# Optimization experiments

Measured on AMD Instinct MI355X. Metric: run time of the kernel, lower is better.

Reference implementation:

```python
import jax, jax.numpy as jnp
import numpy as np

N_NODES = 100000
N_EDGES = 1250000
IN_CH = 64
HID = 64
OUT_CH = 8
N_GRAPHS = 512


def _gcn_conv(x, W, b, src, dst, n):
    """PyG GCNConv: add self-loops, symmetric deg^-1/2 normalization, scatter-add."""
    h = x @ W  # [N, F_out]
    ones = jnp.ones(src.shape, dtype=h.dtype)
    deg = jax.ops.segment_sum(ones, dst, num_segments=n) + 1.0  # +1 for self-loop
    dinv = jax.lax.rsqrt(deg)
    coef = (dinv[src] * dinv[dst])[:, None]          # [E,1]
    agg = jax.ops.segment_sum(h[src] * coef, dst, num_segments=n)  # neighbor msgs
    self_term = h * (dinv * dinv)[:, None]           # self-loop msg, norm = 1/deg
    return agg + self_term + b


def setup_inputs() -> dict:
    key = jax.random.key(0)
    ks = jax.random.split(key, 8)
    x = jax.random.normal(ks[0], (N_NODES, IN_CH), dtype=jnp.float32)
    edge_index = jax.random.randint(ks[1], (2, N_EDGES), 0, N_NODES, dtype=jnp.int64)
    batch = jnp.sort(jax.random.randint(ks[2], (N_NODES,), 0, N_GRAPHS, dtype=jnp.int64))
    s = 0.1
    W0 = jax.random.normal(ks[3], (IN_CH, HID), dtype=jnp.float32) * s
    W1 = jax.random.normal(ks[4], (HID, HID), dtype=jnp.float32) * s
    W2 = jax.random.normal(ks[5], (HID, HID), dtype=jnp.float32) * s
    Wfc = jax.random.normal(ks[6], (HID, OUT_CH), dtype=jnp.float32) * s
    b0 = jnp.zeros((HID,), dtype=jnp.float32)
    b1 = jnp.zeros((HID,), dtype=jnp.float32)
    b2 = jnp.zeros((HID,), dtype=jnp.float32)
    bfc = jnp.zeros((OUT_CH,), dtype=jnp.float32)
    return {"x": x, "edge_index": edge_index, "batch": batch,
            "W0": W0, "b0": b0, "W1": W1, "b1": b1, "W2": W2, "b2": b2,
            "Wfc": Wfc, "bfc": bfc}


def reference(x, edge_index, batch, W0, b0, W1, b1, W2, b2, Wfc, bfc):
    src, dst = edge_index[0], edge_index[1]
    n = x.shape[0]
    h = jax.nn.relu(_gcn_conv(x, W0, b0, src, dst, n))
    h = jax.nn.relu(_gcn_conv(h, W1, b1, src, dst, n))
    h = jax.nn.relu(_gcn_conv(h, W2, b2, src, dst, n))
    # global_mean_pool over graph ids
    sums = jax.ops.segment_sum(h, batch, num_segments=N_GRAPHS)  # [G, HID]
    cnt = jax.ops.segment_sum(jnp.ones((n,), dtype=h.dtype), batch, num_segments=N_GRAPHS)
    pooled = sums / jnp.maximum(cnt, 1.0)[:, None]
    return jax.nn.sigmoid(pooled @ Wfc + bfc)  # [G, OUT_CH]
```

## Files before the change

kernel.cpp:

```cpp
#include <hip/hip_runtime.h>
#include <math.h>


#define FEAT 64
#define CAP 64
#define EDGE_BLOCKS 1024

typedef _Float16 half4 __attribute__((ext_vector_type(4)));
typedef float floatx2 __attribute__((ext_vector_type(2)));


__global__ void k_zero(int* __restrict__ p, int n, float* __restrict__ q, int m) {
    int i = blockIdx.x * blockDim.x + threadIdx.x;
    if (i < n) p[i] = 0;
    if (i < m) q[i] = 0.f;
}


__global__ void k_scatter(const int* __restrict__ ei, int* __restrict__ ecnt,
                          int* __restrict__ csr, int E, int N) {
    int g = blockIdx.x & 7;
    int bi = blockIdx.x >> 3;
    int lo = (int)((long long)N * g >> 3);
    int hi = (int)((long long)N * (g + 1) >> 3);
    for (int base = bi * 1024; base < E; base += (EDGE_BLOCKS / 8) * 1024) {
        int e0 = base + threadIdx.x;
        #pragma unroll
        for (int k = 0; k < 4; ++k) {
            int e = e0 + k * 256;
            if (e < E) {
                int s = ei[e];
                int d = ei[E + e];
                if (d >= lo && d < hi) {
                    int slot = atomicAdd(&ecnt[d], 1);
                    if (slot < CAP) csr[((size_t)d << 6) + slot] = s;
                }
            }
        }
    }
}


template<typename T>
__global__ __launch_bounds__(256, 2)
void k_matmul(const T* __restrict__ X, const float* __restrict__ W,
              const int* __restrict__ ecnt, unsigned int* __restrict__ h8,
              int n) {
    __shared__ float Ws[FEAT][68];
    __shared__ float Xs[FEAT][68];
    int tid = threadIdx.x;
    int cidx = tid & 15;
    int ridx = tid >> 4;
    int rowbase = blockIdx.x << 6;

    const float4* Wg4 = (const float4*)W;
    for (int idx = tid; idx < FEAT * 16; idx += 256) {
        int k = idx >> 4, p = idx & 15;
        *(float4*)&Ws[k][p << 2] = Wg4[idx];
    }
    for (int idx = tid; idx < FEAT * 16; idx += 256) {
        int r = idx >> 4, p = idx & 15;
        int row = rowbase + r;
        float4 v = make_float4(0.f, 0.f, 0.f, 0.f);
        if (row < n) {
            if constexpr (sizeof(T) == 4) {
                v = ((const float4*)X)[(size_t)row * 16 + p];
            } else {
                half4 hv = ((const half4*)X)[(size_t)row * 16 + p];
                v = make_float4((float)hv.x, (float)hv.y, (float)hv.z, (float)hv.w);
            }
        }
        *(float4*)&Xs[r][p << 2] = v;
    }
    __syncthreads();

    int r0 = ridx << 2;
    int c0 = cidx << 2;
    float4 a0 = make_float4(0.f, 0.f, 0.f, 0.f);
    float4 a1 = a0, a2 = a0, a3 = a0;
    #pragma unroll 2
    for (int k = 0; k < FEAT; k += 4) {
        float4 w0 = *(const float4*)&Ws[k + 0][c0];
        float4 w1 = *(const float4*)&Ws[k + 1][c0];
        float4 w2 = *(const float4*)&Ws[k + 2][c0];
        float4 w3 = *(const float4*)&Ws[k + 3][c0];
        float4 x0 = *(const float4*)&Xs[r0 + 0][k];
        float4 x1 = *(const float4*)&Xs[r0 + 1][k];
        float4 x2 = *(const float4*)&Xs[r0 + 2][k];
        float4 x3 = *(const float4*)&Xs[r0 + 3][k];
        a0.x += x0.x*w0.x + x0.y*w1.x + x0.z*w2.x + x0.w*w3.x;
        a0.y += x0.x*w0.y + x0.y*w1.y + x0.z*w2.y + x0.w*w3.y;
        a0.z += x0.x*w0.z + x0.y*w1.z + x0.z*w2.z + x0.w*w3.z;
        a0.w += x0.x*w0.w + x0.y*w1.w + x0.z*w2.w + x0.w*w3.w;
        a1.x += x1.x*w0.x + x1.y*w1.x + x1.z*w2.x + x1.w*w3.x;
        a1.y += x1.x*w0.y + x1.y*w1.y + x1.z*w2.y + x1.w*w3.y;
        a1.z += x1.x*w0.z + x1.y*w1.z + x1.z*w2.z + x1.w*w3.z;
        a1.w += x1.x*w0.w + x1.y*w1.w + x1.z*w2.w + x1.w*w3.w;
        a2.x += x2.x*w0.x + x2.y*w1.x + x2.z*w2.x + x2.w*w3.x;
        a2.y += x2.x*w0.y + x2.y*w1.y + x2.z*w2.y + x2.w*w3.y;
        a2.z += x2.x*w0.z + x2.y*w1.z + x2.z*w2.z + x2.w*w3.z;
        a2.w += x2.x*w0.w + x2.y*w1.w + x2.z*w2.w + x2.w*w3.w;
        a3.x += x3.x*w0.x + x3.y*w1.x + x3.z*w2.x + x3.w*w3.x;
        a3.y += x3.x*w0.y + x3.y*w1.y + x3.z*w2.y + x3.w*w3.y;
        a3.z += x3.x*w0.z + x3.y*w1.z + x3.z*w2.z + x3.w*w3.z;
        a3.w += x3.x*w0.w + x3.y*w1.w + x3.z*w2.w + x3.w*w3.w;
    }
    int row0 = rowbase + r0;
    #pragma unroll
    for (int r = 0; r < 4; ++r) {
        int row = row0 + r;
        if (row < n) {
            float4 a = (r == 0) ? a0 : (r == 1) ? a1 : (r == 2) ? a2 : a3;
            float dv = rsqrtf((float)ecnt[row] + 1.0f);
            unsigned int p = 0;
            p = __builtin_amdgcn_cvt_pk_fp8_f32(a.x * dv, a.y * dv, p, false);
            p = __builtin_amdgcn_cvt_pk_fp8_f32(a.z * dv, a.w * dv, p, true);
            h8[(size_t)row * 16 + cidx] = p;
        }
    }
}


__global__ void k_agg(const int* __restrict__ ecnt, const int* __restrict__ csr,
                      const unsigned int* __restrict__ h8,
                      const float* __restrict__ b, _Float16* __restrict__ out, int N) {
    int wid = (blockIdx.x * blockDim.x + threadIdx.x) >> 6;
    int lane = threadIdx.x & 63;
    int half = lane >> 5;
    int lanein = lane & 31;
    int eslot = lanein >> 4;
    int fq = lanein & 15;
    int node = wid * 2 + half;
    if (node >= N) return;
    int deg = ecnt[node];
    int off0 = node << 6;
    int e1 = off0 + deg;
    float4 acc = make_float4(0.f, 0.f, 0.f, 0.f);
    int j = off0 + eslot;
    for (; j + 2 < e1; j += 4) {
        unsigned int u0 = h8[(size_t)csr[j] * 16 + fq];
        unsigned int u1 = h8[(size_t)csr[j + 2] * 16 + fq];
        floatx2 l0 = __builtin_amdgcn_cvt_pk_f32_fp8(u0, false);
        floatx2 h0 = __builtin_amdgcn_cvt_pk_f32_fp8(u0, true);
        floatx2 l1 = __builtin_amdgcn_cvt_pk_f32_fp8(u1, false);
        floatx2 h1 = __builtin_amdgcn_cvt_pk_f32_fp8(u1, true);
        acc.x += l0.x + l1.x;
        acc.y += l0.y + l1.y;
        acc.z += h0.x + h1.x;
        acc.w += h0.y + h1.y;
    }
    if (j < e1) {
        unsigned int u = h8[(size_t)csr[j] * 16 + fq];
        floatx2 l = __builtin_amdgcn_cvt_pk_f32_fp8(u, false);
        floatx2 hh = __builtin_amdgcn_cvt_pk_f32_fp8(u, true);
        acc.x += l.x; acc.y += l.y; acc.z += hh.x; acc.w += hh.y;
    }
    acc.x += __shfl_xor(acc.x, 16); acc.y += __shfl_xor(acc.y, 16);
    acc.z += __shfl_xor(acc.z, 16); acc.w += __shfl_xor(acc.w, 16);
    if (eslot == 0) {
        unsigned int uo = h8[(size_t)node * 16 + fq];
        floatx2 ol = __builtin_amdgcn_cvt_pk_f32_fp8(uo, false);
        floatx2 oh = __builtin_amdgcn_cvt_pk_f32_fp8(uo, true);
        float4 bb = *(const float4*)&b[fq << 2];
        float dv = rsqrtf((float)deg + 1.0f);
        half4 r;
        r.x = (_Float16)fmaxf(dv * (acc.x + ol.x) + bb.x, 0.f);
        r.y = (_Float16)fmaxf(dv * (acc.y + ol.y) + bb.y, 0.f);
        r.z = (_Float16)fmaxf(dv * (acc.z + oh.x) + bb.z, 0.f);
        r.w = (_Float16)fmaxf(dv * (acc.w + oh.y) + bb.w, 0.f);
        *(half4*)&out[(size_t)node * FEAT + (fq << 2)] = r;
    }
}


#define PCH 64
__global__ void k_pool(const _Float16* __restrict__ h, const int* __restrict__ batch,
                       float* __restrict__ pooled, float* __restrict__ gcnt, int N) {
    int wave = blockIdx.x * (blockDim.x >> 6) + (threadIdx.x >> 6);
    int f = threadIdx.x & 63;
    int start = wave * PCH;
    if (start >= N) return;
    int end = start + PCH; if (end > N) end = N;
    int cur = batch[start];
    float acc = 0.f;
    int nl = 0;
    for (int i = start; i < end; ++i) {
        int g = batch[i];
        if (g != cur) {
            atomicAdd(&pooled[(size_t)cur * FEAT + f], acc);
            if (f == 0) atomicAdd(&gcnt[cur], (float)nl);
            cur = g; acc = 0.f; nl = 0;
        }
        acc += (float)h[(size_t)i * FEAT + f];
        nl++;
    }
    atomicAdd(&pooled[(size_t)cur * FEAT + f], acc);
    if (f == 0) atomicAdd(&gcnt[cur], (float)nl);
}

__global__ void k_fc_sigmoid(const float* __restrict__ pooled, const float* __restrict__ gcnt,
                             const float* __restrict__ Wfc, const float* __restrict__ bfc,
                             float* __restrict__ out, int G) {
    __shared__ float P[FEAT];
    int g = blockIdx.x;
    int t = threadIdx.x;
    float c = fmaxf(gcnt[g], 1.0f);
    P[t] = pooled[(size_t)g * FEAT + t] / c;
    __syncthreads();
    if (t < 8) {
        float acc = bfc[t];
        #pragma unroll
        for (int f = 0; f < FEAT; ++f) acc += P[f] * Wfc[f * 8 + t];
        out[(size_t)g * 8 + t] = 1.f / (1.f + expf(-acc));
    }
}


extern "C" void kernel_launch(void* const* d_in, const int* in_sizes, int n_in,
                              void* d_out, int out_size, void* d_ws, size_t ws_size,
                              hipStream_t stream) {
    const float* x    = (const float*)d_in[0];
    const int*   ei   = (const int*)d_in[1];
    const int*   batch= (const int*)d_in[2];
    const float* W0   = (const float*)d_in[3];
    const float* b0   = (const float*)d_in[4];
    const float* W1   = (const float*)d_in[5];
    const float* b1   = (const float*)d_in[6];
    const float* W2   = (const float*)d_in[7];
    const float* b2   = (const float*)d_in[8];
    const float* Wfc  = (const float*)d_in[9];
    const float* bfc  = (const float*)d_in[10];
    float* out = (float*)d_out;

    const int N = in_sizes[0] / FEAT;
    const int E = in_sizes[1] / 2;
    const int G = out_size / 8;

    _Float16* bufA  = (_Float16*)d_ws;
    _Float16* bufB  = bufA + (size_t)N * FEAT;
    unsigned int* h8 = (unsigned int*)(bufB + (size_t)N * FEAT);
    float* pooled   = (float*)(h8 + (size_t)N * 16);
    float* gcnt     = pooled + (size_t)G * FEAT;
    int*   ecnt     = (int*)(gcnt + G);
    int*   csr      = ecnt + N;

    const int TB = 256;
    dim3 blk(TB);
    dim3 gN((N + TB - 1) / TB);
    dim3 gEP(EDGE_BLOCKS);

    k_zero<<<gN, blk, 0, stream>>>(ecnt, N, pooled, G * (FEAT + 1));
    k_scatter<<<gEP, blk, 0, stream>>>(ei, ecnt, csr, E, N);

    dim3 gAgg(((N + 1) / 2 + 3) / 4);
    dim3 gMM((N + 63) / 64);

    k_matmul<float><<<gMM, blk, 0, stream>>>(x, W0, ecnt, h8, N);
    k_agg<<<gAgg, blk, 0, stream>>>(ecnt, csr, h8, b0, bufA, N);
    k_matmul<_Float16><<<gMM, blk, 0, stream>>>(bufA, W1, ecnt, h8, N);
    k_agg<<<gAgg, blk, 0, stream>>>(ecnt, csr, h8, b1, bufB, N);
    k_matmul<_Float16><<<gMM, blk, 0, stream>>>(bufB, W2, ecnt, h8, N);
    k_agg<<<gAgg, blk, 0, stream>>>(ecnt, csr, h8, b2, bufA, N);

    k_pool<<<dim3(((N + PCH - 1) / PCH + 3) / 4), blk, 0, stream>>>(bufA, batch, pooled, gcnt, N);
    k_fc_sigmoid<<<dim3(G), dim3(FEAT), 0, stream>>>(pooled, gcnt, Wfc, bfc, out, G);
}
```

Measured before the change: 252.5 us.

## Fuse GCN aggregation with next layer's matmul via shared-memory tile

Adds a kernel that, for a 64-node tile, gathers and normalizes each node's neighbour features into shared memory and then multiplies by the next layer's weights, writing FP8 features directly. This replaces two agg+matmul kernel pairs, removing the fp16 intermediate round-trip through global memory and two launches, and ping-pongs between two FP8 buffers. The scatter kernel also loads the source index only for edges whose destination is in range. The trade-off is that each fused block has less latency-hiding parallelism during the irregular gather phase, and 64-node blocks with two nodes per wave per pass may leave the gather underoccupied.

```diff
diff --git a/kernel.cpp b/kernel.cpp
--- a/kernel.cpp
+++ b/kernel.cpp
@@ -29,15 +29,44 @@
         for (int k = 0; k < 4; ++k) {
             int e = e0 + k * 256;
             if (e < E) {
-                int s = ei[e];
                 int d = ei[E + e];
                 if (d >= lo && d < hi) {
+                    int s = ei[e];
                     int slot = atomicAdd(&ecnt[d], 1);
                     if (slot < CAP) csr[((size_t)d << 6) + slot] = s;
                 }
             }
         }
     }
+}
+
+
+__device__ __forceinline__ float4 agg_node(const int* __restrict__ csr,
+                                           const unsigned int* __restrict__ h8,
+                                           int node, int deg, int eslot, int fq) {
+    float4 acc = make_float4(0.f, 0.f, 0.f, 0.f);
+    int off0 = node << 6;
+    int e1 = off0 + deg;
+    int j = off0 + eslot;
+    for (; j + 2 < e1; j += 4) {
+        unsigned int u0 = h8[(size_t)csr[j] * 16 + fq];
+        unsigned int u1 = h8[(size_t)csr[j + 2] * 16 + fq];
+        floatx2 l0 = __builtin_amdgcn_cvt_pk_f32_fp8(u0, false);
+        floatx2 h0 = __builtin_amdgcn_cvt_pk_f32_fp8(u0, true);
+        floatx2 l1 = __builtin_amdgcn_cvt_pk_f32_fp8(u1, false);
+        floatx2 h1 = __builtin_amdgcn_cvt_pk_f32_fp8(u1, true);
+        acc.x += l0.x + l1.x;
+        acc.y += l0.y + l1.y;
+        acc.z += h0.x + h1.x;
+        acc.w += h0.y + h1.y;
+    }
+    if (j < e1) {
+        unsigned int u = h8[(size_t)csr[j] * 16 + fq];
+        floatx2 l = __builtin_amdgcn_cvt_pk_f32_fp8(u, false);
+        floatx2 hh = __builtin_amdgcn_cvt_pk_f32_fp8(u, true);
+        acc.x += l.x; acc.y += l.y; acc.z += hh.x; acc.w += hh.y;
+    }
+    return acc;
 }
 
 
@@ -121,6 +150,106 @@
 }
 
 
+__global__ __launch_bounds__(256, 2)
+void k_agg_mm(const int* __restrict__ ecnt, const int* __restrict__ csr,
+              const unsigned int* __restrict__ h8in, const float* __restrict__ b,
+              const float* __restrict__ W, unsigned int* __restrict__ h8out,
+              int n) {
+    __shared__ float Ws[FEAT][68];
+    __shared__ float Xs[FEAT][68];
+    int tid = threadIdx.x;
+    int rowbase = blockIdx.x << 6;
+
+    const float4* Wg4 = (const float4*)W;
+    for (int idx = tid; idx < FEAT * 16; idx += 256) {
+        int k = idx >> 4, p = idx & 15;
+        *(float4*)&Ws[k][p << 2] = Wg4[idx];
+    }
+
+    int wv = tid >> 6;
+    int lane = tid & 63;
+    int half = lane >> 5;
+    int lanein = lane & 31;
+    int eslot = lanein >> 4;
+    int fq = lanein & 15;
+    for (int p = 0; p < 8; ++p) {
+        int local = wv * 16 + p * 2 + half;
+        int node = rowbase + local;
+        float4 acc = make_float4(0.f, 0.f, 0.f, 0.f);
+        int deg = 0;
+        if (node < n) {
+            deg = ecnt[node];
+            acc = agg_node(csr, h8in, node, deg, eslot, fq);
+        }
+        acc.x += __shfl_xor(acc.x, 16); acc.y += __shfl_xor(acc.y, 16);
+        acc.z += __shfl_xor(acc.z, 16); acc.w += __shfl_xor(acc.w, 16);
+        if (eslot == 0) {
+            float4 r = make_float4(0.f, 0.f, 0.f, 0.f);
+            if (node < n) {
+                unsigned int uo = h8in[(size_t)node * 16 + fq];
+                floatx2 ol = __builtin_amdgcn_cvt_pk_f32_fp8(uo, false);
+                floatx2 oh = __builtin_amdgcn_cvt_pk_f32_fp8(uo, true);
+                float4 bb = *(const float4*)&b[fq << 2];
+                float dv = rsqrtf((float)deg + 1.0f);
+                r.x = fmaxf(dv * (acc.x + ol.x) + bb.x, 0.f);
+                r.y = fmaxf(dv * (acc.y + ol.y) + bb.y, 0.f);
+                r.z = fmaxf(dv * (acc.z + oh.x) + bb.z, 0.f);
+                r.w = fmaxf(dv * (acc.w + oh.y) + bb.w, 0.f);
+            }
+            *(float4*)&Xs[local][fq << 2] = r;
+        }
+    }
+    __syncthreads();
+
+    int cidx = tid & 15;
+    int ridx = tid >> 4;
+    int r0 = ridx << 2;
+    int c0 = cidx << 2;
+    float4 a0 = make_float4(0.f, 0.f, 0.f, 0.f);
+    float4 a1 = a0, a2 = a0, a3 = a0;
+    #pragma unroll 2
+    for (int k = 0; k < FEAT; k += 4) {
+        float4 w0 = *(const float4*)&Ws[k + 0][c0];
+        float4 w1 = *(const float4*)&Ws[k + 1][c0];
+        float4 w2 = *(const float4*)&Ws[k + 2][c0];
+        float4 w3 = *(const float4*)&Ws[k + 3][c0];
+        float4 x0 = *(const float4*)&Xs[r0 + 0][k];
+        float4 x1 = *(const float4*)&Xs[r0 + 1][k];
+        float4 x2 = *(const float4*)&Xs[r0 + 2][k];
+        float4 x3 = *(const float4*)&Xs[r0 + 3][k];
+        a0.x += x0.x*w0.x + x0.y*w1.x + x0.z*w2.x + x0.w*w3.x;
+        a0.y += x0.x*w0.y + x0.y*w1.y + x0.z*w2.y + x0.w*w3.y;
+        a0.z += x0.x*w0.z + x0.y*w1.z + x0.z*w2.z + x0.w*w3.z;
+        a0.w += x0.x*w0.w + x0.y*w1.w + x0.z*w2.w + x0.w*w3.w;
+        a1.x += x1.x*w0.x + x1.y*w1.x + x1.z*w2.x + x1.w*w3.x;
+        a1.y += x1.x*w0.y + x1.y*w1.y + x1.z*w2.y + x1.w*w3.y;
+        a1.z += x1.x*w0.z + x1.y*w1.z + x1.z*w2.z + x1.w*w3.z;
+        a1.w += x1.x*w0.w + x1.y*w1.w + x1.z*w2.w + x1.w*w3.w;
+        a2.x += x2.x*w0.x + x2.y*w1.x + x2.z*w2.x + x2.w*w3.x;
+        a2.y += x2.x*w0.y + x2.y*w1.y + x2.z*w2.y + x2.w*w3.y;
+        a2.z += x2.x*w0.z + x2.y*w1.z + x2.z*w2.z + x2.w*w3.z;
+        a2.w += x2.x*w0.w + x2.y*w1.w + x2.z*w2.w + x2.w*w3.w;
+        a3.x += x3.x*w0.x + x3.y*w1.x + x3.z*w2.x + x3.w*w3.x;
+        a3.y += x3.x*w0.y + x3.y*w1.y + x3.z*w2.y + x3.w*w3.y;
+        a3.z += x3.x*w0.z + x3.y*w1.z + x3.z*w2.z + x3.w*w3.z;
+        a3.w += x3.x*w0.w + x3.y*w1.w + x3.z*w2.w + x3.w*w3.w;
+    }
+    int row0 = rowbase + r0;
+    #pragma unroll
+    for (int r = 0; r < 4; ++r) {
+        int row = row0 + r;
+        if (row < n) {
+            float4 a = (r == 0) ? a0 : (r == 1) ? a1 : (r == 2) ? a2 : a3;
+            float dv = rsqrtf((float)ecnt[row] + 1.0f);
+            unsigned int pk = 0;
+            pk = __builtin_amdgcn_cvt_pk_fp8_f32(a.x * dv, a.y * dv, pk, false);
+            pk = __builtin_amdgcn_cvt_pk_fp8_f32(a.z * dv, a.w * dv, pk, true);
+            h8out[(size_t)row * 16 + cidx] = pk;
+        }
+    }
+}
+
+
 __global__ void k_agg(const int* __restrict__ ecnt, const int* __restrict__ csr,
                       const unsigned int* __restrict__ h8,
                       const float* __restrict__ b, _Float16* __restrict__ out, int N) {
@@ -133,28 +262,7 @@
     int node = wid * 2 + half;
     if (node >= N) return;
     int deg = ecnt[node];
-    int off0 = node << 6;
-    int e1 = off0 + deg;
-    float4 acc = make_float4(0.f, 0.f, 0.f, 0.f);
-    int j = off0 + eslot;
-    for (; j + 2 < e1; j += 4) {
-        unsigned int u0 = h8[(size_t)csr[j] * 16 + fq];
-        unsigned int u1 = h8[(size_t)csr[j + 2] * 16 + fq];
-        floatx2 l0 = __builtin_amdgcn_cvt_pk_f32_fp8(u0, false);
-        floatx2 h0 = __builtin_amdgcn_cvt_pk_f32_fp8(u0, true);
-        floatx2 l1 = __builtin_amdgcn_cvt_pk_f32_fp8(u1, false);
-        floatx2 h1 = __builtin_amdgcn_cvt_pk_f32_fp8(u1, true);
-        acc.x += l0.x + l1.x;
-        acc.y += l0.y + l1.y;
-        acc.z += h0.x + h1.x;
-        acc.w += h0.y + h1.y;
-    }
-    if (j < e1) {
-        unsigned int u = h8[(size_t)csr[j] * 16 + fq];
-        floatx2 l = __builtin_amdgcn_cvt_pk_f32_fp8(u, false);
-        floatx2 hh = __builtin_amdgcn_cvt_pk_f32_fp8(u, true);
-        acc.x += l.x; acc.y += l.y; acc.z += hh.x; acc.w += hh.y;
-    }
+    float4 acc = agg_node(csr, h8, node, deg, eslot, fq);
     acc.x += __shfl_xor(acc.x, 16); acc.y += __shfl_xor(acc.y, 16);
     acc.z += __shfl_xor(acc.z, 16); acc.w += __shfl_xor(acc.w, 16);
     if (eslot == 0) {
@@ -237,9 +345,9 @@
     const int G = out_size / 8;
 
     _Float16* bufA  = (_Float16*)d_ws;
-    _Float16* bufB  = bufA + (size_t)N * FEAT;
-    unsigned int* h8 = (unsigned int*)(bufB + (size_t)N * FEAT);
-    float* pooled   = (float*)(h8 + (size_t)N * 16);
+    unsigned int* h8a = (unsigned int*)(bufA + (size_t)N * FEAT);
+    unsigned int* h8b = h8a + (size_t)N * 16;
+    float* pooled   = (float*)(h8b + (size_t)N * 16);
     float* gcnt     = pooled + (size_t)G * FEAT;
     int*   ecnt     = (int*)(gcnt + G);
     int*   csr      = ecnt + N;
@@ -248,19 +356,16 @@
     dim3 blk(TB);
     dim3 gN((N + TB - 1) / TB);
     dim3 gEP(EDGE_BLOCKS);
+    dim3 gAgg(((N + 1) / 2 + 3) / 4);
+    dim3 gMM((N + 63) / 64);
 
     k_zero<<<gN, blk, 0, stream>>>(ecnt, N, pooled, G * (FEAT + 1));
     k_scatter<<<gEP, blk, 0, stream>>>(ei, ecnt, csr, E, N);
 
-    dim3 gAgg(((N + 1) / 2 + 3) / 4);
-    dim3 gMM((N + 63) / 64);
-
-    k_matmul<float><<<gMM, blk, 0, stream>>>(x, W0, ecnt, h8, N);
-    k_agg<<<gAgg, blk, 0, stream>>>(ecnt, csr, h8, b0, bufA, N);
-    k_matmul<_Float16><<<gMM, blk, 0, stream>>>(bufA, W1, ecnt, h8, N);
-    k_agg<<<gAgg, blk, 0, stream>>>(ecnt, csr, h8, b1, bufB, N);
-    k_matmul<_Float16><<<gMM, blk, 0, stream>>>(bufB, W2, ecnt, h8, N);
-    k_agg<<<gAgg, blk, 0, stream>>>(ecnt, csr, h8, b2, bufA, N);
+    k_matmul<float><<<gMM, blk, 0, stream>>>(x, W0, ecnt, h8a, N);
+    k_agg_mm<<<gMM, blk, 0, stream>>>(ecnt, csr, h8a, b0, W1, h8b, N);
+    k_agg_mm<<<gMM, blk, 0, stream>>>(ecnt, csr, h8b, b1, W2, h8a, N);
+    k_agg<<<gAgg, blk, 0, stream>>>(ecnt, csr, h8a, b2, bufA, N);
 
     k_pool<<<dim3(((N + PCH - 1) / PCH + 3) / 4), blk, 0, stream>>>(bufA, batch, pooled, gcnt, N);
     k_fc_sigmoid<<<dim3(G), dim3(FEAT), 0, stream>>>(pooled, gcnt, Wfc, bfc, out, G);
```

New measurement: 289.6 us. 14.7% more time.

## Use 16 threads per node in aggregation, unroll neighbor gather by four

Applied to the files above, without the earlier changes.

The aggregation kernel now gives each node 16 lanes, with every lane walking all of the node's edges, instead of 32 lanes split across two interleaved edge slots. This removes the cross-lane shuffle reduction and the idle half of the lanes in the epilogue, and unrolls the gather by four to keep more loads in flight per lane. The trade-off is a longer serial loop per lane with fewer nodes per wave in flight relative to edges. The scatter kernel also moves the source-index load behind the destination-range check, so the load is skipped for edges that other blocks own.

```diff
diff --git a/kernel.cpp b/kernel.cpp
--- a/kernel.cpp
+++ b/kernel.cpp
@@ -29,9 +29,9 @@
         for (int k = 0; k < 4; ++k) {
             int e = e0 + k * 256;
             if (e < E) {
-                int s = ei[e];
                 int d = ei[E + e];
                 if (d >= lo && d < hi) {
+                    int s = ei[e];
                     int slot = atomicAdd(&ecnt[d], 1);
                     if (slot < CAP) csr[((size_t)d << 6) + slot] = s;
                 }
@@ -124,52 +124,53 @@
 __global__ void k_agg(const int* __restrict__ ecnt, const int* __restrict__ csr,
                       const unsigned int* __restrict__ h8,
                       const float* __restrict__ b, _Float16* __restrict__ out, int N) {
-    int wid = (blockIdx.x * blockDim.x + threadIdx.x) >> 6;
-    int lane = threadIdx.x & 63;
-    int half = lane >> 5;
-    int lanein = lane & 31;
-    int eslot = lanein >> 4;
-    int fq = lanein & 15;
-    int node = wid * 2 + half;
+    int tid = blockIdx.x * blockDim.x + threadIdx.x;
+    int node = tid >> 4;
+    int fq = tid & 15;
     if (node >= N) return;
     int deg = ecnt[node];
     int off0 = node << 6;
-    int e1 = off0 + deg;
     float4 acc = make_float4(0.f, 0.f, 0.f, 0.f);
-    int j = off0 + eslot;
-    for (; j + 2 < e1; j += 4) {
-        unsigned int u0 = h8[(size_t)csr[j] * 16 + fq];
-        unsigned int u1 = h8[(size_t)csr[j + 2] * 16 + fq];
+    int j = 0;
+    for (; j + 4 <= deg; j += 4) {
+        int s0 = csr[off0 + j];
+        int s1 = csr[off0 + j + 1];
+        int s2 = csr[off0 + j + 2];
+        int s3 = csr[off0 + j + 3];
+        unsigned int u0 = h8[(size_t)s0 * 16 + fq];
+        unsigned int u1 = h8[(size_t)s1 * 16 + fq];
+        unsigned int u2 = h8[(size_t)s2 * 16 + fq];
+        unsigned int u3 = h8[(size_t)s3 * 16 + fq];
         floatx2 l0 = __builtin_amdgcn_cvt_pk_f32_fp8(u0, false);
         floatx2 h0 = __builtin_amdgcn_cvt_pk_f32_fp8(u0, true);
         floatx2 l1 = __builtin_amdgcn_cvt_pk_f32_fp8(u1, false);
         floatx2 h1 = __builtin_amdgcn_cvt_pk_f32_fp8(u1, true);
-        acc.x += l0.x + l1.x;
-        acc.y += l0.y + l1.y;
-        acc.z += h0.x + h1.x;
-        acc.w += h0.y + h1.y;
-    }
-    if (j < e1) {
-        unsigned int u = h8[(size_t)csr[j] * 16 + fq];
+        floatx2 l2 = __builtin_amdgcn_cvt_pk_f32_fp8(u2, false);
+        floatx2 h2 = __builtin_amdgcn_cvt_pk_f32_fp8(u2, true);
+        floatx2 l3 = __builtin_amdgcn_cvt_pk_f32_fp8(u3, false);
+        floatx2 h3 = __builtin_amdgcn_cvt_pk_f32_fp8(u3, true);
+        acc.x += (l0.x + l1.x) + (l2.x + l3.x);
+        acc.y += (l0.y + l1.y) + (l2.y + l3.y);
+        acc.z += (h0.x + h1.x) + (h2.x + h3.x);
+        acc.w += (h0.y + h1.y) + (h2.y + h3.y);
+    }
+    for (; j < deg; ++j) {
+        unsigned int u = h8[(size_t)csr[off0 + j] * 16 + fq];
         floatx2 l = __builtin_amdgcn_cvt_pk_f32_fp8(u, false);
         floatx2 hh = __builtin_amdgcn_cvt_pk_f32_fp8(u, true);
         acc.x += l.x; acc.y += l.y; acc.z += hh.x; acc.w += hh.y;
     }
-    acc.x += __shfl_xor(acc.x, 16); acc.y += __shfl_xor(acc.y, 16);
-    acc.z += __shfl_xor(acc.z, 16); acc.w += __shfl_xor(acc.w, 16);
-    if (eslot == 0) {
-        unsigned int uo = h8[(size_t)node * 16 + fq];
-        floatx2 ol = __builtin_amdgcn_cvt_pk_f32_fp8(uo, false);
-        floatx2 oh = __builtin_amdgcn_cvt_pk_f32_fp8(uo, true);
-        float4 bb = *(const float4*)&b[fq << 2];
-        float dv = rsqrtf((float)deg + 1.0f);
-        half4 r;
-        r.x = (_Float16)fmaxf(dv * (acc.x + ol.x) + bb.x, 0.f);
-        r.y = (_Float16)fmaxf(dv * (acc.y + ol.y) + bb.y, 0.f);
-        r.z = (_Float16)fmaxf(dv * (acc.z + oh.x) + bb.z, 0.f);
-        r.w = (_Float16)fmaxf(dv * (acc.w + oh.y) + bb.w, 0.f);
-        *(half4*)&out[(size_t)node * FEAT + (fq << 2)] = r;
-    }
+    unsigned int uo = h8[(size_t)node * 16 + fq];
+    floatx2 ol = __builtin_amdgcn_cvt_pk_f32_fp8(uo, false);
+    floatx2 oh = __builtin_amdgcn_cvt_pk_f32_fp8(uo, true);
+    float4 bb = *(const float4*)&b[fq << 2];
+    float dv = rsqrtf((float)deg + 1.0f);
+    half4 r;
+    r.x = (_Float16)fmaxf(dv * (acc.x + ol.x) + bb.x, 0.f);
+    r.y = (_Float16)fmaxf(dv * (acc.y + ol.y) + bb.y, 0.f);
+    r.z = (_Float16)fmaxf(dv * (acc.z + oh.x) + bb.z, 0.f);
+    r.w = (_Float16)fmaxf(dv * (acc.w + oh.y) + bb.w, 0.f);
+    *(half4*)&out[(size_t)node * FEAT + (fq << 2)] = r;
 }
 
 
@@ -248,12 +249,11 @@
     dim3 blk(TB);
     dim3 gN((N + TB - 1) / TB);
     dim3 gEP(EDGE_BLOCKS);
+    dim3 gAgg(((size_t)N * 16 + TB - 1) / TB);
+    dim3 gMM((N + 63) / 64);
 
     k_zero<<<gN, blk, 0, stream>>>(ecnt, N, pooled, G * (FEAT + 1));
     k_scatter<<<gEP, blk, 0, stream>>>(ei, ecnt, csr, E, N);
-
-    dim3 gAgg(((N + 1) / 2 + 3) / 4);
-    dim3 gMM((N + 63) / 64);
 
     k_matmul<float><<<gMM, blk, 0, stream>>>(x, W0, ecnt, h8, N);
     k_agg<<<gAgg, blk, 0, stream>>>(ecnt, csr, h8, b0, bufA, N);
```

New measurement: 236.6 us. 6.3% less time.
